# Kernel tuning notes

Measured on AMD Instinct MI355X. Metric: run time of the kernel, lower is better.

Reference implementation:

```python
import jax, jax.numpy as jnp
import numpy as np
import math

B, D, H, W, C = 1, 16, 56, 56, 256
WD, WH, WW = 2, 7, 7
NH, NP = 8, 4
N = WD * WH * WW          # 98 tokens per window
HD = C // NH
NWIN = (D // WD) * (H // WH) * (W // WW)  # 512


def layernorm(x, g, b, eps=1e-5):
    m = x.mean(-1, keepdims=True)
    v = jnp.mean((x - m) ** 2, -1, keepdims=True)
    return (x - m) * jax.lax.rsqrt(v + eps) * g + b


def _reference_points():
    zz = (jnp.arange(WD, dtype=jnp.float32) + 0.5) / WD
    yy = (jnp.arange(WH, dtype=jnp.float32) + 0.5) / WH
    xx = (jnp.arange(WW, dtype=jnp.float32) + 0.5) / WW
    gz, gy, gx = jnp.meshgrid(zz, yy, xx, indexing='ij')
    return jnp.stack([gx.ravel(), gy.ravel(), gz.ravel()], -1)  # (N, 3) in xyz order


def _trilinear(value, loc):
    # value: (Bn, N, NH, HD); loc: (Bn, N, NH, NP, 3) normalized xyz in [0,1]
    # grid_sample semantics: align_corners=False, zero padding
    Bn = value.shape[0]
    v = value.transpose(0, 2, 1, 3)  # (Bn, NH, S, HD), S == N (window volume)
    px = loc[..., 0] * WW - 0.5
    py = loc[..., 1] * WH - 0.5
    pz = loc[..., 2] * WD - 0.5
    x0, y0, z0 = jnp.floor(px), jnp.floor(py), jnp.floor(pz)
    out = jnp.zeros(loc.shape[:-1] + (HD,), value.dtype)
    for dz in (0, 1):
        for dy in (0, 1):
            for dx in (0, 1):
                xi, yi, zi = x0 + dx, y0 + dy, z0 + dz
                wgt = (1 - jnp.abs(px - xi)) * (1 - jnp.abs(py - yi)) * (1 - jnp.abs(pz - zi))
                valid = ((xi >= 0) & (xi < WW) & (yi >= 0) & (yi < WH) & (zi >= 0) & (zi < WD)).astype(value.dtype)
                idx = (jnp.clip(zi, 0, WD - 1) * (WH * WW) + jnp.clip(yi, 0, WH - 1) * WW
                       + jnp.clip(xi, 0, WW - 1)).astype(jnp.int32)  # (Bn, N, NH, NP)
                idxf = idx.transpose(0, 2, 1, 3).reshape(Bn, NH, N * NP)
                g = jnp.take_along_axis(v, idxf[..., None], axis=2)  # (Bn, NH, N*NP, HD)
                g = g.reshape(Bn, NH, N, NP, HD).transpose(0, 2, 1, 3, 4)
                out = out + g * (wgt * valid)[..., None]
    return out  # (Bn, N, NH, NP, HD)


def setup_inputs():
    key = jax.random.key(0)
    ks = jax.random.split(key, 12)

    def lin(k, fin, fout):
        s = 1.0 / np.sqrt(fin)
        kw, kb = jax.random.split(k)
        return (jax.random.uniform(kw, (fin, fout), jnp.float32, -s, s),
                jax.random.uniform(kb, (fout,), jnp.float32, -s, s))

    val_w, val_b = lin(ks[2], C, C)
    off_w, off_b = lin(ks[3], C, NH * NP * 3)
    aw_w, aw_b = lin(ks[4], C, NH * NP)
    out_w, out_b = lin(ks[5], C, C)
    proj_w, proj_b = lin(ks[6], C, C)
    fc1_w, fc1_b = lin(ks[7], C, 4 * C)
    fc2_w, fc2_b = lin(ks[8], 4 * C, C)
    return dict(
        x=jax.random.normal(ks[0], (B, D, H, W, C), jnp.float32),
        mask=jax.random.uniform(ks[1], (NWIN, N, WD, WH, WW), jnp.float32),
        norm1_g=jnp.ones((C,), jnp.float32), norm1_b=jnp.zeros((C,), jnp.float32),
        val_w=val_w, val_b=val_b, off_w=off_w, off_b=off_b,
        aw_w=aw_w, aw_b=aw_b, out_w=out_w, out_b=out_b,
        anorm_g=jnp.ones((C,), jnp.float32), anorm_b=jnp.zeros((C,), jnp.float32),
        proj_w=proj_w, proj_b=proj_b,
        norm2_g=jnp.ones((C,), jnp.float32), norm2_b=jnp.zeros((C,), jnp.float32),
        fc1_w=fc1_w, fc1_b=fc1_b, fc2_w=fc2_w, fc2_b=fc2_b)


def reference(x, mask, norm1_g, norm1_b, val_w, val_b, off_w, off_b, aw_w, aw_b,
              out_w, out_b, anorm_g, anorm_b, proj_w, proj_b,
              norm2_g, norm2_b, fc1_w, fc1_b, fc2_w, fc2_b):
    shortcut = x
    xn = layernorm(x, norm1_g, norm1_b)
    # window partition (dims divisible by window, shift_size = 0 -> no pad/roll)
    xw = xn.reshape(B, D // WD, WD, H // WH, WH, W // WW, WW, C)
    xw = xw.transpose(0, 1, 3, 5, 2, 4, 6, 7).reshape(-1, N, C)  # (B*NWIN, N, C)
    Bn = B * NWIN
    # --- PositionEmbeddingSine over the per-window mask ---
    z_e = jnp.cumsum(mask, 2) * mask / math.pi
    y_e = jnp.cumsum(mask, 3) * mask / math.pi
    x_e = jnp.cumsum(mask, 4) * mask / math.pi
    emb = mask * (jnp.sin(x_e) + jnp.sin(math.pi * y_e) + z_e)
    emb = emb.reshape(NWIN, N, N)  # flatten(2); N == WD*WH*WW
    diag = jnp.diagonal(emb, axis1=1, axis2=2)  # (NWIN, N)
    q = (xw.reshape(B, NWIN, N, C) + diag[None, :, :, None]).reshape(Bn, N, C)
    # --- MS3DDeformAttn over single level = window ---
    ref = _reference_points()  # (N, 3)
    value = (xw @ val_w + val_b).reshape(Bn, N, NH, HD)
    off = (q @ off_w + off_b).reshape(Bn, N, NH, NP, 3)
    aw = jax.nn.softmax((q @ aw_w + aw_b).reshape(Bn, N, NH, NP), axis=-1)
    loc = ref[None, :, None, None, :] + off / jnp.array([WW, WH, WD], jnp.float32)
    sampled = _trilinear(value, loc)                       # (Bn, N, NH, NP, HD)
    attn = (sampled * aw[..., None]).sum(3).reshape(Bn, N, C) @ out_w + out_b
    # WindowAttention3D epilogue: proj(norm(x + attn))
    xw = layernorm(xw + attn, anorm_g, anorm_b) @ proj_w + proj_b
    # window reverse
    xr = xw.reshape(B, D // WD, H // WH, W // WW, WD, WH, WW, C)
    xr = xr.transpose(0, 1, 4, 2, 5, 3, 6, 7).reshape(B, D, H, W, C)
    x = shortcut + xr
    # MLP branch
    h = layernorm(x, norm2_g, norm2_b)
    h = jax.nn.gelu(h @ fc1_w + fc1_b)
    return x + (h @ fc2_w + fc2_b)
```

## Files before the change

### kernel.cpp

```cpp
#include <hip/hip_runtime.h>
#include <hip/hip_bf16.h>
#include <hip/hip_fp16.h>

#define B2F(x) __bfloat162float(x)
#define F2B(x) __float2bfloat16(x)

typedef __bf16 bf16x8 __attribute__((ext_vector_type(8)));
typedef float floatx4 __attribute__((ext_vector_type(4)));

static constexpr int MROWS = 50176;
static constexpr int CDIM  = 256;

enum { MODE_BF16 = 0, MODE_VALOFFAW = 1 };

#if defined(__has_builtin)
#if __has_builtin(__builtin_amdgcn_global_load_lds)
#define HAS_GLL 1
#endif
#endif
#ifndef HAS_GLL
#define HAS_GLL 0
#endif


__device__ __forceinline__ void win_decode(int r, int& tok) {
    int w = r / 98, n = r - w * 98;
    int dB = w >> 6, hB = (w >> 3) & 7, wB = w & 7;
    int z = n / 49, n2 = n - z * 49, yy = n2 / 7, xx = n2 - yy * 7;
    tok = ((dB * 2 + z) * 56 + hB * 7 + yy) * 56 + wB * 7 + xx;
}

__device__ __forceinline__ float bf2f(unsigned short u) {
    return __uint_as_float(((unsigned)u) << 16);
}

__device__ __forceinline__ float wave_sum64(float v) {
#pragma unroll
    for (int off = 32; off > 0; off >>= 1) v += __shfl_xor(v, off, 64);
    return v;
}


__global__ __launch_bounds__(256) void fused_pre(
    const float* __restrict__ x, const float* __restrict__ n1g, const float* __restrict__ n1b,
    __hip_bfloat16* __restrict__ xw,
    const float* __restrict__ mask, float* __restrict__ diag, float* __restrict__ csum,
    const float* __restrict__ val_w, const float* __restrict__ off_w,
    const float* __restrict__ aw_w,  const float* __restrict__ out_w,
    const float* __restrict__ proj_w, const float* __restrict__ fc1_w,
    const float* __restrict__ fc2_w,
    __hip_bfloat16* __restrict__ valT, __hip_bfloat16* __restrict__ offawT,
    __hip_bfloat16* __restrict__ outT, __hip_bfloat16* __restrict__ projT,
    __hip_bfloat16* __restrict__ fc1T, __hip_bfloat16* __restrict__ fc2T) {
    const int bid = blockIdx.x;
    const int tid = threadIdx.x;

    if (bid < 2944) {
        const float* src; __hip_bfloat16* dst; int K, N, base;
        if (bid < 256)       { src = val_w;  dst = valT;            K = 256;  N = 256;  base = 0; }
        else if (bid < 352)  { src = off_w;  dst = offawT;          K = 256;  N = 96;   base = 256; }
        else if (bid < 384)  { src = aw_w;   dst = offawT + 96*256; K = 256;  N = 32;   base = 352; }
        else if (bid < 640)  { src = out_w;  dst = outT;            K = 256;  N = 256;  base = 384; }
        else if (bid < 896)  { src = proj_w; dst = projT;           K = 256;  N = 256;  base = 640; }
        else if (bid < 1920) { src = fc1_w;  dst = fc1T;            K = 256;  N = 1024; base = 896; }
        else                 { src = fc2_w;  dst = fc2T;            K = 1024; N = 256;  base = 1920; }
        int i = (bid - base) * 256 + tid;
        if (i >= K * N) return;
        int nn = i / K, kk = i - nn * K;
        dst[(size_t)nn * K + kk] = F2B(src[(size_t)kk * N + nn]);
    } else if (bid < 3140) {
        int r = (bid - 2944) * 256 + tid;
        int n = r % 98;
        int z = n / 49, n2 = n - z * 49, yy = n2 / 7, xx = n2 - yy * 7;
        const float* mb = mask + (size_t)r * 98;
        float m = mb[z * 49 + yy * 7 + xx];
        float sz = 0.f, sy = 0.f, sx = 0.f;
        for (int k = 0; k <= z; ++k)  sz += mb[k * 49 + yy * 7 + xx];
        for (int k = 0; k <= yy; ++k) sy += mb[z * 49 + k * 7 + xx];
        for (int k = 0; k <= xx; ++k) sx += mb[z * 49 + yy * 7 + k];
        const float PI = 3.14159265358979323846f;
        diag[r] = m * (sinf(sx * m / PI) + sinf(sy * m) + sz * m / PI);
    } else if (bid == 3140) {
        if (tid < 96) {
            float s = 0.f;
            for (int k = 0; k < 256; ++k) s += off_w[(size_t)k * 96 + tid];
            csum[tid] = s;
        } else if (tid < 128) {
            int n = tid - 96;
            float s = 0.f;
            for (int k = 0; k < 256; ++k) s += aw_w[(size_t)k * 32 + n];
            csum[tid] = s;
        }
    } else {
        const int lane = tid & 63;
        const int rb = (bid - 3141) * 16 + (tid >> 6) * 4;
        const int c0 = lane * 4;
        float4 v[4];
#pragma unroll
        for (int k = 0; k < 4; ++k) {
            int tok; win_decode(rb + k, tok);
            v[k] = *(const float4*)(x + (size_t)tok * CDIM + c0);
        }
        float4 gg = *(const float4*)(n1g + c0);
        float4 bb = *(const float4*)(n1b + c0);
#pragma unroll
        for (int k = 0; k < 4; ++k) {
            float mean = wave_sum64(v[k].x + v[k].y + v[k].z + v[k].w) * (1.f / 256.f);
            float dx = v[k].x - mean, dy = v[k].y - mean, dz = v[k].z - mean, dw = v[k].w - mean;
            float var = wave_sum64(dx * dx + dy * dy + dz * dz + dw * dw) * (1.f / 256.f);
            float rstd = rsqrtf(var + 1e-5f);
            __hip_bfloat16 ob[4] = { F2B(dx * rstd * gg.x + bb.x), F2B(dy * rstd * gg.y + bb.y),
                                     F2B(dz * rstd * gg.z + bb.z), F2B(dw * rstd * gg.w + bb.w) };
            *(ushort4*)(xw + (size_t)(rb + k) * CDIM + c0) = *(const ushort4*)ob;
        }
    }
}


__global__ __launch_bounds__(512, 4) void sample_fused(
    const __half* __restrict__ offaw,
    const __hip_bfloat16* __restrict__ value,
    __hip_bfloat16* __restrict__ ai) {
    __shared__ __align__(16) __hip_bfloat16 vs[98 * 256];
    __shared__ __align__(16) __half os[98 * 128];
    const int tid = threadIdx.x;
    const int w = blockIdx.x;

#if HAS_GLL
    {
        const uint4* vsrc = (const uint4*)(value + (size_t)w * 98 * CDIM);
#pragma unroll
        for (int k = 0; k < 7; ++k) {
            int i = tid + k * 512;
            if (i < 3136)
                __builtin_amdgcn_global_load_lds(
                    (const __attribute__((address_space(1))) void*)(vsrc + i),
                    (__attribute__((address_space(3))) void*)(((uint4*)vs) + i), 16, 0, 0);
        }
        const uint4* osrc = (const uint4*)(offaw + (size_t)w * 98 * 128);
#pragma unroll
        for (int k = 0; k < 4; ++k) {
            int i = tid + k * 512;
            if (i < 1568)
                __builtin_amdgcn_global_load_lds(
                    (const __attribute__((address_space(1))) void*)(osrc + i),
                    (__attribute__((address_space(3))) void*)(((uint4*)os) + i), 16, 0, 0);
        }
    }
#else
    {
        const uint4* vsrc = (const uint4*)(value + (size_t)w * 98 * CDIM);
        uint4* vdst = (uint4*)vs;
        for (int i = tid; i < 3136; i += 512) vdst[i] = vsrc[i];
        const uint4* osrc = (const uint4*)(offaw + (size_t)w * 98 * 128);
        uint4* odst = (uint4*)os;
        for (int i = tid; i < 1568; i += 512) odst[i] = osrc[i];
    }
#endif
    __syncthreads();

    const int lane  = tid & 63;
    const int wave  = tid >> 6;
    const int h     = lane >> 3;
    const int s     = lane & 7;
    const int p     = s >> 1;
    const int jbase = (s & 1) * 4;
    const int boff  = lane * 8;
    const int gbase = lane & ~7;

    for (int r = wave; r < 98; r += 8) {
        int z = r / 49, n2 = r - z * 49, yy = n2 / 7, xx = n2 - yy * 7;
        const __half* orow = os + r * 128;

        float l0 = __half2float(orow[96 + h * 4 + 0]);
        float l1 = __half2float(orow[96 + h * 4 + 1]);
        float l2 = __half2float(orow[96 + h * 4 + 2]);
        float l3 = __half2float(orow[96 + h * 4 + 3]);
        float mx = fmaxf(fmaxf(l0, l1), fmaxf(l2, l3));
        float e0 = __expf(l0 - mx), e1 = __expf(l1 - mx), e2 = __expf(l2 - mx), e3 = __expf(l3 - mx);
        float inv = 1.f / (e0 + e1 + e2 + e3);
        float ep = (p == 0) ? e0 : (p == 1) ? e1 : (p == 2) ? e2 : e3;
        float wp = ep * inv;

        float ox = __half2float(orow[h * 12 + p * 3 + 0]);
        float oy = __half2float(orow[h * 12 + p * 3 + 1]);
        float oz = __half2float(orow[h * 12 + p * 3 + 2]);
        float px = (float)xx + ox, py = (float)yy + oy, pz = (float)z + oz;
        float fx0 = floorf(px), fy0 = floorf(py), fz0 = floorf(pz);
        int ix = (int)fx0, iy = (int)fy0, iz = (int)fz0;
        float fx = px - fx0, fy = py - fy0, fz = pz - fz0;

        uint packed[4];
#pragma unroll
        for (int jj = 0; jj < 4; ++jj) {
            int j = jbase + jj;
            int dzz = j >> 2, dyy = (j >> 1) & 1, dxx = j & 1;
            int zi = iz + dzz, yi = iy + dyy, xi = ix + dxx;
            float wz = dzz ? fz : 1.f - fz;
            float wy = dyy ? fy : 1.f - fy;
            float wxw = dxx ? fx : 1.f - fx;
            bool valid = (zi >= 0) & (zi < 2) & (yi >= 0) & (yi < 7) & (xi >= 0) & (xi < 7);
            float wc = valid ? wp * wz * wy * wxw : 0.f;
            int zc = min(max(zi, 0), 1), yc = min(max(yi, 0), 6), xc = min(max(xi, 0), 6);
            int idx = zc * 49 + yc * 7 + xc;
            packed[jj] = ((uint)(idx * 512) << 16) | (uint)__half_as_ushort(__float2half(wc));
        }

        float a0 = 0.f, a1 = 0.f, a2 = 0.f, a3 = 0.f;
#pragma unroll
        for (int jj = 0; jj < 4; ++jj) {
            uint mine = packed[jj];
#pragma unroll
            for (int sl = 0; sl < 8; ++sl) {
                uint pk = __shfl(mine, gbase + sl, 64);
                float wj = __half2float(__ushort_as_half((unsigned short)(pk & 0xffffu)));
                ushort4 v = *(const ushort4*)((const char*)vs + (pk >> 16) + boff);
                a0 += wj * bf2f(v.x);
                a1 += wj * bf2f(v.y);
                a2 += wj * bf2f(v.z);
                a3 += wj * bf2f(v.w);
            }
        }
        __hip_bfloat16 ob[4] = { F2B(a0), F2B(a1), F2B(a2), F2B(a3) };
        *(ushort4*)(ai + ((size_t)w * 98 + r) * CDIM + lane * 4) = *(const ushort4*)ob;
    }
}


template <int MODE>
__global__ __launch_bounds__(256) void gemm_bt(
    const __hip_bfloat16* __restrict__ A,
    const __hip_bfloat16* __restrict__ Bt,
    const int N, const int K,
    const float* __restrict__ bias0,
    const float* __restrict__ bias1,
    const float* __restrict__ bias2,
    void* C,
    void* extra,
    const void* extra2,
    const float* __restrict__ csum) {
    __shared__ __align__(16) __hip_bfloat16 As[2][128 * 32];
    __shared__ __align__(16) __hip_bfloat16 Bs[2][128 * 32];
    const int tid  = threadIdx.x;
    const int lane = tid & 63;
    const int wave = tid >> 6;
    const int wm = (wave >> 1) * 64;
    const int wn = (wave & 1) * 64;
    const int row0 = blockIdx.x * 128;
    const int col0 = blockIdx.y * 128;
    const int l15 = lane & 15;
    const int quad = lane >> 4;

    floatx4 acc[4][4] = {};

    const int sr = tid >> 2;
    const int sk = (tid & 3) * 8;

    const __hip_bfloat16* Ab = A + (size_t)row0 * K + sr * (size_t)K + sk;
    const __hip_bfloat16* Bb = Bt + (size_t)col0 * K + sr * (size_t)K + sk;
    const size_t half64 = (size_t)64 * K;

    auto stage = [&](int buf, int k0) {
#if HAS_GLL
        __builtin_amdgcn_global_load_lds(
            (const __attribute__((address_space(1))) void*)(Ab + k0),
            (__attribute__((address_space(3))) void*)(&As[buf][sr * 32 + sk]), 16, 0, 0);
        __builtin_amdgcn_global_load_lds(
            (const __attribute__((address_space(1))) void*)(Ab + half64 + k0),
            (__attribute__((address_space(3))) void*)(&As[buf][(sr + 64) * 32 + sk]), 16, 0, 0);
        __builtin_amdgcn_global_load_lds(
            (const __attribute__((address_space(1))) void*)(Bb + k0),
            (__attribute__((address_space(3))) void*)(&Bs[buf][sr * 32 + sk]), 16, 0, 0);
        __builtin_amdgcn_global_load_lds(
            (const __attribute__((address_space(1))) void*)(Bb + half64 + k0),
            (__attribute__((address_space(3))) void*)(&Bs[buf][(sr + 64) * 32 + sk]), 16, 0, 0);
#else
        *reinterpret_cast<uint4*>(&As[buf][sr * 32 + sk]) = *reinterpret_cast<const uint4*>(Ab + k0);
        *reinterpret_cast<uint4*>(&As[buf][(sr + 64) * 32 + sk]) = *reinterpret_cast<const uint4*>(Ab + half64 + k0);
        *reinterpret_cast<uint4*>(&Bs[buf][sr * 32 + sk]) = *reinterpret_cast<const uint4*>(Bb + k0);
        *reinterpret_cast<uint4*>(&Bs[buf][(sr + 64) * 32 + sk]) = *reinterpret_cast<const uint4*>(Bb + half64 + k0);
#endif
    };

    const int nk = K >> 5;
    stage(0, 0);
    for (int t = 0; t < nk; ++t) {
        __syncthreads();
        if (t + 1 < nk) stage((t + 1) & 1, (t + 1) * 32);
        const __hip_bfloat16* Asb = As[t & 1];
        const __hip_bfloat16* Bsb = Bs[t & 1];
        bf16x8 af[4], bfg[4];
#pragma unroll
        for (int i = 0; i < 4; ++i)
            af[i] = *reinterpret_cast<const bf16x8*>(&Asb[(wm + i * 16 + l15) * 32 + quad * 8]);
#pragma unroll
        for (int j = 0; j < 4; ++j)
            bfg[j] = *reinterpret_cast<const bf16x8*>(&Bsb[(wn + j * 16 + l15) * 32 + quad * 8]);
#pragma unroll
        for (int i = 0; i < 4; ++i)
#pragma unroll
            for (int j = 0; j < 4; ++j)
                acc[i][j] = __builtin_amdgcn_mfma_f32_16x16x32_bf16(af[i], bfg[j], acc[i][j], 0, 0, 0);
    }

#pragma unroll
    for (int i = 0; i < 4; ++i) {
#pragma unroll
        for (int j = 0; j < 4; ++j) {
#pragma unroll
            for (int rr = 0; rr < 4; ++rr) {
                int row = row0 + wm + i * 16 + quad * 4 + rr;
                int col = col0 + wn + j * 16 + l15;
                float v = acc[i][j][rr];
                if constexpr (MODE == MODE_BF16) {
                    v += bias0[col];
                    ((__hip_bfloat16*)C)[(size_t)row * N + col] = F2B(v);
                } else {
                    if (col < 256) {
                        v += bias0[col];
                        ((__hip_bfloat16*)C)[(size_t)row * 256 + col] = F2B(v);
                    } else {
                        int c2 = col - 256;
                        const float* diag = (const float*)extra2;
                        v += (c2 < 96 ? bias1[c2] : bias2[c2 - 96]);
                        v += diag[row] * csum[c2];
                        ((__half*)extra)[(size_t)row * 128 + c2] = __float2half(v);
                    }
                }
            }
        }
    }
}


template <int REV>
__global__ __launch_bounds__(512, 4) void gemm_row_ln(
    const __hip_bfloat16* __restrict__ A,
    const __hip_bfloat16* __restrict__ Bt,
    const float* __restrict__ bias,
    const __hip_bfloat16* __restrict__ xw,
    const float* __restrict__ xf,
    const float* __restrict__ g, const float* __restrict__ b,
    __hip_bfloat16* __restrict__ obf,
    float* __restrict__ of32) {
    __shared__ __align__(16) __hip_bfloat16 As[2][128 * 32];
    __shared__ __align__(16) __hip_bfloat16 Bs[2][256 * 32];
    __shared__ float p1[128 * 4], p2[128 * 4];
    const int tid  = threadIdx.x;
    const int lane = tid & 63;
    const int w    = tid >> 6;
    const int l15  = lane & 15;
    const int quad = lane >> 4;
    const int wm   = (w >> 2) * 64;
    const int wn   = (w & 3) * 64;
    const int wc   = w & 3;
    const int row0 = blockIdx.x * 128;

    const int sr = tid >> 2;
    const int sk = (tid & 3) * 8;
    const __hip_bfloat16* Ab = A + (size_t)(row0 + sr) * 256 + sk;
    const __hip_bfloat16* Bb = Bt + (size_t)sr * 256 + sk;

    floatx4 acc[4][4] = {};

    auto stage = [&](int buf, int k0) {
#if HAS_GLL
        __builtin_amdgcn_global_load_lds(
            (const __attribute__((address_space(1))) void*)(Ab + k0),
            (__attribute__((address_space(3))) void*)(&As[buf][sr * 32 + sk]), 16, 0, 0);
        __builtin_amdgcn_global_load_lds(
            (const __attribute__((address_space(1))) void*)(Bb + k0),
            (__attribute__((address_space(3))) void*)(&Bs[buf][sr * 32 + sk]), 16, 0, 0);
        __builtin_amdgcn_global_load_lds(
            (const __attribute__((address_space(1))) void*)(Bb + (size_t)128 * 256 + k0),
            (__attribute__((address_space(3))) void*)(&Bs[buf][(sr + 128) * 32 + sk]), 16, 0, 0);
#else
        *reinterpret_cast<uint4*>(&As[buf][sr * 32 + sk]) = *reinterpret_cast<const uint4*>(Ab + k0);
        *reinterpret_cast<uint4*>(&Bs[buf][sr * 32 + sk]) = *reinterpret_cast<const uint4*>(Bb + k0);
        *reinterpret_cast<uint4*>(&Bs[buf][(sr + 128) * 32 + sk]) = *reinterpret_cast<const uint4*>(Bb + (size_t)128 * 256 + k0);
#endif
    };

    stage(0, 0);
    for (int t = 0; t < 8; ++t) {
        __syncthreads();
        if (t + 1 < 8) stage((t + 1) & 1, (t + 1) * 32);
        const __hip_bfloat16* Asb = As[t & 1];
        const __hip_bfloat16* Bsb = Bs[t & 1];
        bf16x8 af[4], bfg[4];
#pragma unroll
        for (int i = 0; i < 4; ++i)
            af[i] = *reinterpret_cast<const bf16x8*>(&Asb[(wm + i * 16 + l15) * 32 + quad * 8]);
#pragma unroll
        for (int j = 0; j < 4; ++j)
            bfg[j] = *reinterpret_cast<const bf16x8*>(&Bsb[(wn + j * 16 + l15) * 32 + quad * 8]);
#pragma unroll
        for (int i = 0; i < 4; ++i)
#pragma unroll
            for (int j = 0; j < 4; ++j)
                acc[i][j] = __builtin_amdgcn_mfma_f32_16x16x32_bf16(af[i], bfg[j], acc[i][j], 0, 0, 0);
    }

    float biasj[4], gj[4], bj[4];
#pragma unroll
    for (int j = 0; j < 4; ++j) {
        int col = wn + j * 16 + l15;
        biasj[j] = bias[col];
        gj[j] = g[col];
        bj[j] = b[col];
    }

#pragma unroll
    for (int i = 0; i < 4; ++i) {
#pragma unroll
        for (int rr = 0; rr < 4; ++rr) {
            int lrow = wm + i * 16 + quad * 4 + rr;
            int grow = row0 + lrow;
            int tok = 0;
            if (REV) win_decode(grow, tok);
            float s1 = 0.f, s2 = 0.f;
#pragma unroll
            for (int j = 0; j < 4; ++j) {
                int col = wn + j * 16 + l15;
                float v = acc[i][j][rr] + biasj[j];
                if constexpr (REV == 0) {
                    v += B2F(xw[(size_t)grow * 256 + col]);
                } else {
                    v += xf[(size_t)tok * 256 + col];
                    of32[(size_t)tok * 256 + col] = v;
                }
                acc[i][j][rr] = v;
                s1 += v;
                s2 += v * v;
            }
#pragma unroll
            for (int off = 1; off < 16; off <<= 1) {
                s1 += __shfl_xor(s1, off, 64);
                s2 += __shfl_xor(s2, off, 64);
            }
            if (l15 == 0) {
                p1[lrow * 4 + wc] = s1;
                p2[lrow * 4 + wc] = s2;
            }
        }
    }
    __syncthreads();

#pragma unroll
    for (int i = 0; i < 4; ++i) {
#pragma unroll
        for (int rr = 0; rr < 4; ++rr) {
            int lrow = wm + i * 16 + quad * 4 + rr;
            int grow = row0 + lrow;
            int tok = 0;
            if (REV) win_decode(grow, tok);
            float t1 = p1[lrow * 4 + 0] + p1[lrow * 4 + 1] + p1[lrow * 4 + 2] + p1[lrow * 4 + 3];
            float t2 = p2[lrow * 4 + 0] + p2[lrow * 4 + 1] + p2[lrow * 4 + 2] + p2[lrow * 4 + 3];
            float mean = t1 * (1.f / 256.f);
            float var = t2 * (1.f / 256.f) - mean * mean;
            float rstd = rsqrtf(var + 1e-5f);
            size_t orow = REV ? (size_t)tok : (size_t)grow;
#pragma unroll
            for (int j = 0; j < 4; ++j) {
                int col = wn + j * 16 + l15;
                float o = (acc[i][j][rr] - mean) * rstd * gj[j] + bj[j];
                obf[orow * 256 + col] = F2B(o);
            }
        }
    }
}


__global__ __launch_bounds__(512, 4) void mlp_fused(
    const __hip_bfloat16* __restrict__ hin,
    const __hip_bfloat16* __restrict__ fc1T,
    const __hip_bfloat16* __restrict__ fc2T,
    const float* __restrict__ fc1_b, const float* __restrict__ fc2_b,
    float* __restrict__ out) {
    __shared__ __align__(16) __hip_bfloat16 hs[8 * 128 * 32];
    __shared__ __align__(16) __hip_bfloat16 as[2 * 128 * 32];
    const int tid  = threadIdx.x;
    const int lane = tid & 63;
    const int w    = tid >> 6;
    const int r0   = blockIdx.x * 128;
    const int l15  = lane & 15;
    const int quad = lane >> 4;
    const int wm   = (w >> 2) * 64;
    const int wn   = (w & 3) * 64;
    const int ac   = (w & 3) * 16;

    {
        const int row = tid >> 2, ke = (tid & 3) * 8;
#if HAS_GLL
#pragma unroll
        for (int kt = 0; kt < 8; ++kt)
            __builtin_amdgcn_global_load_lds(
                (const __attribute__((address_space(1))) void*)(hin + (size_t)(r0 + row) * 256 + kt * 32 + ke),
                (__attribute__((address_space(3))) void*)(&hs[kt * 4096 + row * 32 + ke]), 16, 0, 0);
#else
#pragma unroll
        for (int kt = 0; kt < 8; ++kt)
            *(uint4*)(&hs[kt * 4096 + row * 32 + ke]) =
                *(const uint4*)(hin + (size_t)(r0 + row) * 256 + kt * 32 + ke);
#endif
    }
    floatx4 acc[4][4] = {};
    const int kt2 = (ac + l15) >> 5, ko = (ac + l15) & 31;
    __syncthreads();

    for (int kk = 0; kk < 1024; kk += 64) {
        floatx4 pa[4] = {};
#pragma unroll
        for (int ks = 0; ks < 8; ++ks) {
            bf16x8 b1 = *(const bf16x8*)(fc1T + (size_t)(kk + ac + l15) * 256 + ks * 32 + quad * 8);
#pragma unroll
            for (int i = 0; i < 4; ++i) {
                bf16x8 a = *(const bf16x8*)(&hs[ks * 4096 + (wm + i * 16 + l15) * 32 + quad * 8]);
                pa[i] = __builtin_amdgcn_mfma_f32_16x16x32_bf16(a, b1, pa[i], 0, 0, 0);
            }
        }
        float bb = fc1_b[kk + ac + l15];
        __syncthreads();
#pragma unroll
        for (int i = 0; i < 4; ++i) {
#pragma unroll
            for (int rr = 0; rr < 4; ++rr) {
                float v = pa[i][rr] + bb;
                float t2 = 1.5957691216057308f * (v + 0.044715f * v * v * v);
                v = v / (1.f + __expf(-t2));
                int row = wm + i * 16 + quad * 4 + rr;
                as[kt2 * 4096 + row * 32 + ko] = F2B(v);
            }
        }
        __syncthreads();
#pragma unroll
        for (int ks = 0; ks < 2; ++ks) {
            bf16x8 a4[4];
#pragma unroll
            for (int i = 0; i < 4; ++i)
                a4[i] = *(const bf16x8*)(&as[ks * 4096 + (wm + i * 16 + l15) * 32 + quad * 8]);
#pragma unroll
            for (int j = 0; j < 4; ++j) {
                bf16x8 b2 = *(const bf16x8*)(fc2T + (size_t)(wn + j * 16 + l15) * 1024 + kk + ks * 32 + quad * 8);
#pragma unroll
                for (int i = 0; i < 4; ++i)
                    acc[i][j] = __builtin_amdgcn_mfma_f32_16x16x32_bf16(a4[i], b2, acc[i][j], 0, 0, 0);
            }
        }
    }
#pragma unroll
    for (int i = 0; i < 4; ++i)
#pragma unroll
        for (int j = 0; j < 4; ++j)
#pragma unroll
            for (int rr = 0; rr < 4; ++rr) {
                int row = r0 + wm + i * 16 + quad * 4 + rr;
                int col = wn + j * 16 + l15;
                out[(size_t)row * 256 + col] += acc[i][j][rr] + fc2_b[col];
            }
}


extern "C" void kernel_launch(void* const* d_in, const int* in_sizes, int n_in,
                              void* d_out, int out_size, void* d_ws, size_t ws_size,
                              hipStream_t stream) {
    const float* x      = (const float*)d_in[0];
    const float* mask   = (const float*)d_in[1];
    const float* n1g    = (const float*)d_in[2];
    const float* n1b    = (const float*)d_in[3];
    const float* val_w  = (const float*)d_in[4];
    const float* val_b  = (const float*)d_in[5];
    const float* off_w  = (const float*)d_in[6];
    const float* off_b  = (const float*)d_in[7];
    const float* aw_w   = (const float*)d_in[8];
    const float* aw_b   = (const float*)d_in[9];
    const float* out_w  = (const float*)d_in[10];
    const float* out_b  = (const float*)d_in[11];
    const float* ang    = (const float*)d_in[12];
    const float* anb    = (const float*)d_in[13];
    const float* proj_w = (const float*)d_in[14];
    const float* proj_b = (const float*)d_in[15];
    const float* n2g    = (const float*)d_in[16];
    const float* n2b    = (const float*)d_in[17];
    const float* fc1_w  = (const float*)d_in[18];
    const float* fc1_b  = (const float*)d_in[19];
    const float* fc2_w  = (const float*)d_in[20];
    const float* fc2_b  = (const float*)d_in[21];

    char* ws = (char*)d_ws;
    size_t o = 0;
    auto alloc = [&](size_t bytes) {
        size_t r = o;
        o += (bytes + 255) & ~(size_t)255;
        return r;
    };
    const size_t M = MROWS;
    const size_t REGION_B = M * 128 * 2 + M * 256 * 2;

    __hip_bfloat16* valT    = (__hip_bfloat16*)(ws + alloc(256 * 256 * 2));
    __hip_bfloat16* offawT  = (__hip_bfloat16*)(ws + alloc(128 * 256 * 2));
    __hip_bfloat16* outT    = (__hip_bfloat16*)(ws + alloc(256 * 256 * 2));
    __hip_bfloat16* projT   = (__hip_bfloat16*)(ws + alloc(256 * 256 * 2));
    __hip_bfloat16* fc1T    = (__hip_bfloat16*)(ws + alloc(1024 * 256 * 2));
    __hip_bfloat16* fc2T    = (__hip_bfloat16*)(ws + alloc(256 * 1024 * 2));
    float*          csum    = (float*)(ws + alloc(128 * 4));
    float*          diag    = (float*)(ws + alloc(M * 4));
    char*           slab1   = ws + alloc(M * 256 * 2);
    char*           region  = ws + alloc(REGION_B);
    (void)ws_size; (void)in_sizes; (void)n_in; (void)out_size;

    __hip_bfloat16* xw    = (__hip_bfloat16*)slab1;
    __hip_bfloat16* a2    = (__hip_bfloat16*)slab1;
    __half*         offaw = (__half*)region;
    __hip_bfloat16* ai    = (__hip_bfloat16*)(region + M * 128 * 2);
    __hip_bfloat16* hin   = (__hip_bfloat16*)region;
    __hip_bfloat16* value = (__hip_bfloat16*)d_out;
    float*          xres  = (float*)d_out;

    dim3 blk(256);
    hipLaunchKernelGGL(fused_pre, dim3(2944 + 196 + 1 + MROWS / 16), blk, 0, stream,
                       x, n1g, n1b, xw, mask, diag, csum,
                       val_w, off_w, aw_w, out_w, proj_w, fc1_w, fc2_w,
                       valT, offawT, outT, projT, fc1T, fc2T);
    hipLaunchKernelGGL((gemm_bt<MODE_VALOFFAW>), dim3(MROWS / 128, 3), blk, 0, stream,
                       xw, valT, 384, 256, val_b, off_b, aw_b,
                       (void*)value, (void*)offaw, (const void*)diag, csum);
    hipLaunchKernelGGL(sample_fused, dim3(MROWS / 98), dim3(512), 0, stream,
                       offaw, value, ai);
    hipLaunchKernelGGL((gemm_row_ln<0>), dim3(MROWS / 128), dim3(512), 0, stream,
                       ai, outT, out_b, xw, (const float*)nullptr, ang, anb,
                       a2, (float*)nullptr);
    hipLaunchKernelGGL((gemm_row_ln<1>), dim3(MROWS / 128), dim3(512), 0, stream,
                       a2, projT, proj_b, (const __hip_bfloat16*)nullptr, x, n2g, n2b,
                       hin, xres);
    hipLaunchKernelGGL(mlp_fused, dim3(MROWS / 128), dim3(512), 0, stream,
                       hin, fc1T, fc2T, fc1_b, fc2_b, (float*)d_out);
}
```

Baseline: 451.6 us.

## Fuse proj GEMM with norm2 LayerNorm into the MLP kernel

Merges the proj GEMM, residual add, window reverse and norm2 LayerNorm (formerly gemm_row_ln<1>) into the MLP kernel. The normalized tile is written straight into LDS as the fc1 input, so the bf16 hin round trip through global memory and one kernel launch go away. The residual output is written and accumulated using window-decoded token rows. The cost is a larger 80KB shared buffer per block, which may lower occupancy, and scattered row writes in the MLP epilogue.

```diff
diff --git a/kernel.cpp b/kernel.cpp
--- a/kernel.cpp
+++ b/kernel.cpp
@@ -333,16 +333,13 @@
 }
 
 
-template <int REV>
 __global__ __launch_bounds__(512, 4) void gemm_row_ln(
     const __hip_bfloat16* __restrict__ A,
     const __hip_bfloat16* __restrict__ Bt,
     const float* __restrict__ bias,
     const __hip_bfloat16* __restrict__ xw,
-    const float* __restrict__ xf,
     const float* __restrict__ g, const float* __restrict__ b,
-    __hip_bfloat16* __restrict__ obf,
-    float* __restrict__ of32) {
+    __hip_bfloat16* __restrict__ obf) {
     __shared__ __align__(16) __hip_bfloat16 As[2][128 * 32];
     __shared__ __align__(16) __hip_bfloat16 Bs[2][256 * 32];
     __shared__ float p1[128 * 4], p2[128 * 4];
@@ -416,19 +413,11 @@
         for (int rr = 0; rr < 4; ++rr) {
             int lrow = wm + i * 16 + quad * 4 + rr;
             int grow = row0 + lrow;
-            int tok = 0;
-            if (REV) win_decode(grow, tok);
             float s1 = 0.f, s2 = 0.f;
 #pragma unroll
             for (int j = 0; j < 4; ++j) {
                 int col = wn + j * 16 + l15;
-                float v = acc[i][j][rr] + biasj[j];
-                if constexpr (REV == 0) {
-                    v += B2F(xw[(size_t)grow * 256 + col]);
-                } else {
-                    v += xf[(size_t)tok * 256 + col];
-                    of32[(size_t)tok * 256 + col] = v;
-                }
+                float v = acc[i][j][rr] + biasj[j] + B2F(xw[(size_t)grow * 256 + col]);
                 acc[i][j][rr] = v;
                 s1 += v;
                 s2 += v * v;
@@ -452,61 +441,161 @@
         for (int rr = 0; rr < 4; ++rr) {
             int lrow = wm + i * 16 + quad * 4 + rr;
             int grow = row0 + lrow;
-            int tok = 0;
-            if (REV) win_decode(grow, tok);
             float t1 = p1[lrow * 4 + 0] + p1[lrow * 4 + 1] + p1[lrow * 4 + 2] + p1[lrow * 4 + 3];
             float t2 = p2[lrow * 4 + 0] + p2[lrow * 4 + 1] + p2[lrow * 4 + 2] + p2[lrow * 4 + 3];
             float mean = t1 * (1.f / 256.f);
             float var = t2 * (1.f / 256.f) - mean * mean;
             float rstd = rsqrtf(var + 1e-5f);
-            size_t orow = REV ? (size_t)tok : (size_t)grow;
 #pragma unroll
             for (int j = 0; j < 4; ++j) {
                 int col = wn + j * 16 + l15;
                 float o = (acc[i][j][rr] - mean) * rstd * gj[j] + bj[j];
-                obf[orow * 256 + col] = F2B(o);
-            }
-        }
-    }
-}
-
-
-__global__ __launch_bounds__(512, 4) void mlp_fused(
-    const __hip_bfloat16* __restrict__ hin,
+                obf[(size_t)grow * 256 + col] = F2B(o);
+            }
+        }
+    }
+}
+
+
+__global__ __launch_bounds__(512, 4) void mlp_fused_ln(
+    const __hip_bfloat16* __restrict__ A,
+    const __hip_bfloat16* __restrict__ Bt,
+    const float* __restrict__ bias,
+    const float* __restrict__ xf,
+    const float* __restrict__ g, const float* __restrict__ b,
     const __hip_bfloat16* __restrict__ fc1T,
     const __hip_bfloat16* __restrict__ fc2T,
     const float* __restrict__ fc1_b, const float* __restrict__ fc2_b,
-    float* __restrict__ out) {
-    __shared__ __align__(16) __hip_bfloat16 hs[8 * 128 * 32];
-    __shared__ __align__(16) __hip_bfloat16 as[2 * 128 * 32];
+    float* __restrict__ of32) {
+    __shared__ __align__(16) char smem[81920];
+    __hip_bfloat16* As0 = (__hip_bfloat16*)smem;
+    __hip_bfloat16* Bs0 = (__hip_bfloat16*)(smem + 16384);
+    float* p1 = (float*)(smem + 65536);
+    float* p2 = (float*)(smem + 65536 + 2048);
+    __hip_bfloat16* hs  = (__hip_bfloat16*)smem;
+    __hip_bfloat16* as_ = (__hip_bfloat16*)(smem + 65536);
+
     const int tid  = threadIdx.x;
     const int lane = tid & 63;
     const int w    = tid >> 6;
-    const int r0   = blockIdx.x * 128;
     const int l15  = lane & 15;
     const int quad = lane >> 4;
     const int wm   = (w >> 2) * 64;
     const int wn   = (w & 3) * 64;
-    const int ac   = (w & 3) * 16;
-
-    {
-        const int row = tid >> 2, ke = (tid & 3) * 8;
+    const int wc   = w & 3;
+    const int row0 = blockIdx.x * 128;
+
+    const int sr = tid >> 2;
+    const int sk = (tid & 3) * 8;
+    const __hip_bfloat16* Ab = A + (size_t)(row0 + sr) * 256 + sk;
+    const __hip_bfloat16* Bb = Bt + (size_t)sr * 256 + sk;
+
+    floatx4 acc[4][4] = {};
+
+    auto stage = [&](int buf, int k0) {
 #if HAS_GLL
-#pragma unroll
-        for (int kt = 0; kt < 8; ++kt)
-            __builtin_amdgcn_global_load_lds(
-                (const __attribute__((address_space(1))) void*)(hin + (size_t)(r0 + row) * 256 + kt * 32 + ke),
-                (__attribute__((address_space(3))) void*)(&hs[kt * 4096 + row * 32 + ke]), 16, 0, 0);
+        __builtin_amdgcn_global_load_lds(
+            (const __attribute__((address_space(1))) void*)(Ab + k0),
+            (__attribute__((address_space(3))) void*)(&As0[buf * 4096 + sr * 32 + sk]), 16, 0, 0);
+        __builtin_amdgcn_global_load_lds(
+            (const __attribute__((address_space(1))) void*)(Bb + k0),
+            (__attribute__((address_space(3))) void*)(&Bs0[buf * 8192 + sr * 32 + sk]), 16, 0, 0);
+        __builtin_amdgcn_global_load_lds(
+            (const __attribute__((address_space(1))) void*)(Bb + (size_t)128 * 256 + k0),
+            (__attribute__((address_space(3))) void*)(&Bs0[buf * 8192 + (sr + 128) * 32 + sk]), 16, 0, 0);
 #else
-#pragma unroll
-        for (int kt = 0; kt < 8; ++kt)
-            *(uint4*)(&hs[kt * 4096 + row * 32 + ke]) =
-                *(const uint4*)(hin + (size_t)(r0 + row) * 256 + kt * 32 + ke);
+        *reinterpret_cast<uint4*>(&As0[buf * 4096 + sr * 32 + sk]) = *reinterpret_cast<const uint4*>(Ab + k0);
+        *reinterpret_cast<uint4*>(&Bs0[buf * 8192 + sr * 32 + sk]) = *reinterpret_cast<const uint4*>(Bb + k0);
+        *reinterpret_cast<uint4*>(&Bs0[buf * 8192 + (sr + 128) * 32 + sk]) = *reinterpret_cast<const uint4*>(Bb + (size_t)128 * 256 + k0);
 #endif
-    }
-    floatx4 acc[4][4] = {};
+    };
+
+    stage(0, 0);
+    for (int t = 0; t < 8; ++t) {
+        __syncthreads();
+        if (t + 1 < 8) stage((t + 1) & 1, (t + 1) * 32);
+        const __hip_bfloat16* Asb = &As0[(t & 1) * 4096];
+        const __hip_bfloat16* Bsb = &Bs0[(t & 1) * 8192];
+        bf16x8 af[4], bfg[4];
+#pragma unroll
+        for (int i = 0; i < 4; ++i)
+            af[i] = *reinterpret_cast<const bf16x8*>(&Asb[(wm + i * 16 + l15) * 32 + quad * 8]);
+#pragma unroll
+        for (int j = 0; j < 4; ++j)
+            bfg[j] = *reinterpret_cast<const bf16x8*>(&Bsb[(wn + j * 16 + l15) * 32 + quad * 8]);
+#pragma unroll
+        for (int i = 0; i < 4; ++i)
+#pragma unroll
+            for (int j = 0; j < 4; ++j)
+                acc[i][j] = __builtin_amdgcn_mfma_f32_16x16x32_bf16(af[i], bfg[j], acc[i][j], 0, 0, 0);
+    }
+
+    float biasj[4], gj[4], bj[4];
+#pragma unroll
+    for (int j = 0; j < 4; ++j) {
+        int col = wn + j * 16 + l15;
+        biasj[j] = bias[col];
+        gj[j] = g[col];
+        bj[j] = b[col];
+    }
+    int toks[4][4];
+#pragma unroll
+    for (int i = 0; i < 4; ++i) {
+#pragma unroll
+        for (int rr = 0; rr < 4; ++rr) {
+            int lrow = wm + i * 16 + quad * 4 + rr;
+            int tok; win_decode(row0 + lrow, tok);
+            toks[i][rr] = tok;
+            float s1 = 0.f, s2 = 0.f;
+#pragma unroll
+            for (int j = 0; j < 4; ++j) {
+                int col = wn + j * 16 + l15;
+                float v = acc[i][j][rr] + biasj[j] + xf[(size_t)tok * 256 + col];
+                of32[(size_t)tok * 256 + col] = v;
+                acc[i][j][rr] = v;
+                s1 += v;
+                s2 += v * v;
+            }
+#pragma unroll
+            for (int off = 1; off < 16; off <<= 1) {
+                s1 += __shfl_xor(s1, off, 64);
+                s2 += __shfl_xor(s2, off, 64);
+            }
+            if (l15 == 0) {
+                p1[lrow * 4 + wc] = s1;
+                p2[lrow * 4 + wc] = s2;
+            }
+        }
+    }
+    __syncthreads();
+
+#pragma unroll
+    for (int i = 0; i < 4; ++i) {
+#pragma unroll
+        for (int rr = 0; rr < 4; ++rr) {
+            int lrow = wm + i * 16 + quad * 4 + rr;
+            float t1 = p1[lrow * 4 + 0] + p1[lrow * 4 + 1] + p1[lrow * 4 + 2] + p1[lrow * 4 + 3];
+            float t2 = p2[lrow * 4 + 0] + p2[lrow * 4 + 1] + p2[lrow * 4 + 2] + p2[lrow * 4 + 3];
+            float mean = t1 * (1.f / 256.f);
+            float var = t2 * (1.f / 256.f) - mean * mean;
+            float rstd = rsqrtf(var + 1e-5f);
+#pragma unroll
+            for (int j = 0; j < 4; ++j) {
+                int col = wn + j * 16 + l15;
+                float o = (acc[i][j][rr] - mean) * rstd * gj[j] + bj[j];
+                hs[(col >> 5) * 4096 + lrow * 32 + (col & 31)] = F2B(o);
+            }
+        }
+    }
+    __syncthreads();
+
+#pragma unroll
+    for (int i = 0; i < 4; ++i)
+#pragma unroll
+        for (int j = 0; j < 4; ++j)
+            acc[i][j] = floatx4{0.f, 0.f, 0.f, 0.f};
+    const int ac = (w & 3) * 16;
     const int kt2 = (ac + l15) >> 5, ko = (ac + l15) & 31;
-    __syncthreads();
 
     for (int kk = 0; kk < 1024; kk += 64) {
         floatx4 pa[4] = {};
@@ -529,7 +618,7 @@
                 float t2 = 1.5957691216057308f * (v + 0.044715f * v * v * v);
                 v = v / (1.f + __expf(-t2));
                 int row = wm + i * 16 + quad * 4 + rr;
-                as[kt2 * 4096 + row * 32 + ko] = F2B(v);
+                as_[kt2 * 4096 + row * 32 + ko] = F2B(v);
             }
         }
         __syncthreads();
@@ -538,7 +627,7 @@
             bf16x8 a4[4];
 #pragma unroll
             for (int i = 0; i < 4; ++i)
-                a4[i] = *(const bf16x8*)(&as[ks * 4096 + (wm + i * 16 + l15) * 32 + quad * 8]);
+                a4[i] = *(const bf16x8*)(&as_[ks * 4096 + (wm + i * 16 + l15) * 32 + quad * 8]);
 #pragma unroll
             for (int j = 0; j < 4; ++j) {
                 bf16x8 b2 = *(const bf16x8*)(fc2T + (size_t)(wn + j * 16 + l15) * 1024 + kk + ks * 32 + quad * 8);
@@ -554,9 +643,9 @@
         for (int j = 0; j < 4; ++j)
 #pragma unroll
             for (int rr = 0; rr < 4; ++rr) {
-                int row = r0 + wm + i * 16 + quad * 4 + rr;
+                int tok = toks[i][rr];
                 int col = wn + j * 16 + l15;
-                out[(size_t)row * 256 + col] += acc[i][j][rr] + fc2_b[col];
+                of32[(size_t)tok * 256 + col] += acc[i][j][rr] + fc2_b[col];
             }
 }
 
@@ -613,7 +702,6 @@
     __hip_bfloat16* a2    = (__hip_bfloat16*)slab1;
     __half*         offaw = (__half*)region;
     __hip_bfloat16* ai    = (__hip_bfloat16*)(region + M * 128 * 2);
-    __hip_bfloat16* hin   = (__hip_bfloat16*)region;
     __hip_bfloat16* value = (__hip_bfloat16*)d_out;
     float*          xres  = (float*)d_out;
 
@@ -627,12 +715,9 @@
                        (void*)value, (void*)offaw, (const void*)diag, csum);
     hipLaunchKernelGGL(sample_fused, dim3(MROWS / 98), dim3(512), 0, stream,
                        offaw, value, ai);
-    hipLaunchKernelGGL((gemm_row_ln<0>), dim3(MROWS / 128), dim3(512), 0, stream,
-                       ai, outT, out_b, xw, (const float*)nullptr, ang, anb,
-                       a2, (float*)nullptr);
-    hipLaunchKernelGGL((gemm_row_ln<1>), dim3(MROWS / 128), dim3(512), 0, stream,
-                       a2, projT, proj_b, (const __hip_bfloat16*)nullptr, x, n2g, n2b,
-                       hin, xres);
-    hipLaunchKernelGGL(mlp_fused, dim3(MROWS / 128), dim3(512), 0, stream,
-                       hin, fc1T, fc2T, fc1_b, fc2_b, (float*)d_out);
-}
+    hipLaunchKernelGGL(gemm_row_ln, dim3(MROWS / 128), dim3(512), 0, stream,
+                       ai, outT, out_b, xw, ang, anb, a2);
+    hipLaunchKernelGGL(mlp_fused_ln, dim3(MROWS / 128), dim3(512), 0, stream,
+                       a2, projT, proj_b, x, n2g, n2b,
+                       fc1T, fc2T, fc1_b, fc2_b, xres);
+}
```

After: 454.4 us. Within noise of the previous version (+0.6%).
